# Optimization experiments

Measured on AMD Instinct MI355X. Metric: run time of the kernel, lower is better.

Reference implementation:

```python
import jax, jax.numpy as jnp
import numpy as np

EPS = 1e-6
NUM_HEADS = 16


def _layernorm(x, g, b):
    m = jnp.mean(x, axis=-1, keepdims=True)
    v = jnp.mean(jnp.square(x - m), axis=-1, keepdims=True)
    return (x - m) / jnp.sqrt(v + EPS) * g + b


def _rotate_half(x):
    x1, x2 = jnp.split(x, 2, axis=-1)
    return jnp.concatenate([-x2, x1], axis=-1)


def setup_inputs() -> dict:
    key = jax.random.key(0)
    B, N, C = 2, 2048, 1024
    H = NUM_HEADS
    D = C // H
    F = int(C * 4.0)
    ks = jax.random.split(key, 12)
    s = 0.02
    pos = jnp.arange(N)[:, None].astype(jnp.float32)
    inv_freq = 1.0 / (10000.0 ** (jnp.arange(0, D, 2, dtype=jnp.float32) / D))
    freqs = pos * inv_freq[None, :]          # [N, D/2]
    emb = jnp.concatenate([freqs, freqs], axis=-1)  # [N, D]
    return {
        "x": jax.random.normal(ks[0], (B, N, C), jnp.float32),
        "rotary_cos": jnp.cos(emb),
        "rotary_sin": jnp.sin(emb),
        "ln1_g": jnp.ones((C,), jnp.float32),
        "ln1_b": jnp.zeros((C,), jnp.float32),
        "Wq": jax.random.normal(ks[1], (C, C), jnp.float32) * s,
        "bq": jnp.zeros((C,), jnp.float32),
        "Wk": jax.random.normal(ks[2], (C, C), jnp.float32) * s,
        "bk": jnp.zeros((C,), jnp.float32),
        "Wv": jax.random.normal(ks[3], (C, C), jnp.float32) * s,
        "bv": jnp.zeros((C,), jnp.float32),
        "Wo": jax.random.normal(ks[4], (C, C), jnp.float32) * s,
        "bo": jnp.zeros((C,), jnp.float32),
        "ln2_g": jnp.ones((C,), jnp.float32),
        "ln2_b": jnp.zeros((C,), jnp.float32),
        "W1": jax.random.normal(ks[5], (F, C), jnp.float32) * s,
        "b1": jnp.zeros((F,), jnp.float32),
        "W2": jax.random.normal(ks[6], (C, F), jnp.float32) * s,
        "b2": jnp.zeros((C,), jnp.float32),
    }


def reference(x, rotary_cos, rotary_sin, ln1_g, ln1_b, Wq, bq, Wk, bk, Wv, bv,
              Wo, bo, ln2_g, ln2_b, W1, b1, W2, b2):
    B, N, C = x.shape
    H = NUM_HEADS
    D = C // H

    # --- attention branch ---
    h = _layernorm(x, ln1_g, ln1_b)
    q = (h @ Wq.T + bq).reshape(B, N, H, D).transpose(0, 2, 1, 3)  # [B,H,N,D]
    k = (h @ Wk.T + bk).reshape(B, N, H, D).transpose(0, 2, 1, 3)
    v = (h @ Wv.T + bv).reshape(B, N, H, D).transpose(0, 2, 1, 3)

    cos = rotary_cos[None, None, :, :]  # [1,1,N,D]
    sin = rotary_sin[None, None, :, :]
    q = q * cos + _rotate_half(q) * sin
    k = k * cos + _rotate_half(k) * sin

    scale = D ** -0.5
    attn = jnp.einsum('bhnd,bhmd->bhnm', q, k) * scale
    attn = jax.nn.softmax(attn, axis=-1)
    out = jnp.einsum('bhnm,bhmd->bhnd', attn, v)
    out = out.transpose(0, 2, 1, 3).reshape(B, N, C)
    out = out @ Wo.T + bo
    x = x + out

    # --- MLP branch ---
    h = _layernorm(x, ln2_g, ln2_b)
    h = jax.nn.gelu(h @ W1.T + b1, approximate=False)  # torch nn.GELU exact
    h = h @ W2.T + b2
    return x + h
```

## Files before the change

### kernel.cpp

```cpp
#include <hip/hip_runtime.h>
#include <hip/hip_bf16.h>

#define B_ 2
#define N_ 2048
#define C_ 1024
#define H_ 16
#define D_ 64
#define F_ 4096
#define M_ 4096

typedef __attribute__((ext_vector_type(8))) short bf16x8;
typedef __attribute__((ext_vector_type(4))) float f32x4;

__device__ inline unsigned short f2bf(float f) {
  unsigned int u = __float_as_uint(f);
  u = (u + 0x7FFFu + ((u >> 16) & 1u)) >> 16;
  return (unsigned short)u;
}

__global__ __launch_bounds__(256)
void cvt_all(const float4* __restrict__ s0, const float4* __restrict__ s1,
             const float4* __restrict__ s2, const float4* __restrict__ s3,
             const float4* __restrict__ s4, const float4* __restrict__ s5,
             ushort4* __restrict__ d0, ushort4* __restrict__ d1,
             ushort4* __restrict__ d2, ushort4* __restrict__ d3,
             ushort4* __restrict__ d4, ushort4* __restrict__ d5) {
  int b = blockIdx.x;
  const float4* s; ushort4* d; int i;
  if      (b < 1024) { s = s0; d = d0; i = b * 256 + threadIdx.x; }
  else if (b < 2048) { s = s1; d = d1; i = (b - 1024) * 256 + threadIdx.x; }
  else if (b < 3072) { s = s2; d = d2; i = (b - 2048) * 256 + threadIdx.x; }
  else if (b < 4096) { s = s3; d = d3; i = (b - 3072) * 256 + threadIdx.x; }
  else if (b < 8192) { s = s4; d = d4; i = (b - 4096) * 256 + threadIdx.x; }
  else               { s = s5; d = d5; i = (b - 8192) * 256 + threadIdx.x; }
  float4 f = s[i];
  ushort4 o;
  o.x = f2bf(f.x); o.y = f2bf(f.y); o.z = f2bf(f.z); o.w = f2bf(f.w);
  d[i] = o;
}

__global__ __launch_bounds__(256)
void ln_kernel(const float* __restrict__ x, const float* __restrict__ g,
               const float* __restrict__ b, unsigned short* __restrict__ out) {
  __shared__ float red[8];
  const int row = blockIdx.x;
  const int t = threadIdx.x;
  const float4 xv = *(const float4*)(x + row * 1024 + t * 4);
  float s  = xv.x + xv.y + xv.z + xv.w;
  float sq = xv.x * xv.x + xv.y * xv.y + xv.z * xv.z + xv.w * xv.w;
  #pragma unroll
  for (int off = 32; off >= 1; off >>= 1) {
    s  += __shfl_down(s, off);
    sq += __shfl_down(sq, off);
  }
  const int lane = t & 63, wave = t >> 6;
  if (lane == 0) { red[wave * 2] = s; red[wave * 2 + 1] = sq; }
  __syncthreads();
  float ts = red[0] + red[2] + red[4] + red[6];
  float tq = red[1] + red[3] + red[5] + red[7];
  float mean = ts * (1.0f / 1024.0f);
  float var  = tq * (1.0f / 1024.0f) - mean * mean;
  float rstd = rsqrtf(var + 1e-6f);
  float xs[4] = {xv.x, xv.y, xv.z, xv.w};
  #pragma unroll
  for (int i = 0; i < 4; i++) {
    int c = t * 4 + i;
    float y = (xs[i] - mean) * rstd * g[c] + b[c];
    out[row * 1024 + c] = f2bf(y);
  }
}

template<int MODE, int BN>
__global__ __launch_bounds__(256)
void gemm_bt(const unsigned short* __restrict__ A,
             const unsigned short* __restrict__ Bw,
             int K, int Nout, int npc,
             const float* __restrict__ bias,
             const float* __restrict__ resid,
             unsigned short* __restrict__ out_bf,
             float* __restrict__ out_f32) {
  constexpr int NJ = BN / 32;
  __shared__ unsigned short sA[128 * 64];
  __shared__ unsigned short sB[BN * 64];
  const int t = threadIdx.x;
  const int wave = t >> 6, lane = t & 63;
  const int quad = lane >> 4, l16 = lane & 15;
  const int wm = (wave & 1) * 64, wn = (wave >> 1) * (BN / 2);
  const int id = blockIdx.y * gridDim.x + blockIdx.x;
  const int xcd = id & 7, r_ = id >> 3;
  const int n_blk = xcd * npc + r_ % npc;
  const int m_blk = r_ / npc;
  const int m0 = m_blk * 128, n0 = n_blk * BN;

  f32x4 acc[4][NJ];
  #pragma unroll
  for (int i = 0; i < 4; i++)
    #pragma unroll
    for (int j = 0; j < NJ; j++) acc[i][j] = (f32x4){0.f, 0.f, 0.f, 0.f};

  const unsigned short* gA = A  + (m0 + (t >> 3)) * K + (t & 7) * 8;
  const unsigned short* gB = Bw + (n0 + (t >> 3)) * K + (t & 7) * 8;
  unsigned short* lA = &sA[(wave * 8) * 64];
  unsigned short* lB = &sB[(wave * 8) * 64];

  for (int k0 = 0; k0 < K; k0 += 64) {
    #pragma unroll
    for (int i = 0; i < 4; i++)
      __builtin_amdgcn_global_load_lds((const unsigned int*)(gA + (32 * i) * K + k0),
                                       (unsigned int*)(lA + 32 * i * 64), 16, 0, 0);
    #pragma unroll
    for (int i = 0; i < BN / 32; i++)
      __builtin_amdgcn_global_load_lds((const unsigned int*)(gB + (32 * i) * K + k0),
                                       (unsigned int*)(lB + 32 * i * 64), 16, 0, 0);
    __syncthreads();
    #pragma unroll
    for (int kk = 0; kk < 2; kk++) {
      bf16x8 af[4], bfr[NJ];
      #pragma unroll
      for (int i = 0; i < 4; i++)
        af[i] = *(const bf16x8*)(&sA[(wm + i * 16 + l16) * 64 + kk * 32 + quad * 8]);
      #pragma unroll
      for (int j = 0; j < NJ; j++)
        bfr[j] = *(const bf16x8*)(&sB[(wn + j * 16 + l16) * 64 + kk * 32 + quad * 8]);
      #pragma unroll
      for (int i = 0; i < 4; i++)
        #pragma unroll
        for (int j = 0; j < NJ; j++)
          acc[i][j] = __builtin_amdgcn_mfma_f32_16x16x32_bf16(af[i], bfr[j], acc[i][j], 0, 0, 0);
    }
    __syncthreads();
  }

  #pragma unroll
  for (int i = 0; i < 4; i++) {
    #pragma unroll
    for (int j = 0; j < NJ; j++) {
      int col = n0 + wn + j * 16 + l16;
      #pragma unroll
      for (int r = 0; r < 4; r++) {
        int row = m0 + wm + i * 16 + quad * 4 + r;
        float v = acc[i][j][r];
        if (MODE == 1 || MODE == 3) {
          out_f32[row * Nout + col] = v + bias[col] + resid[row * Nout + col];
        } else {
          v += bias[col];
          float w = v * (1.0f + 0.044715f * v * v);
          float gl = v / (1.0f + __expf(-1.5957691216f * w));
          out_bf[row * Nout + col] = f2bf(gl);
        }
      }
    }
  }
}

__global__ __launch_bounds__(256)
void gemm_qkv(const unsigned short* __restrict__ A,
              const unsigned short* __restrict__ Bw,
              const float* __restrict__ bq, const float* __restrict__ bk,
              const float* __restrict__ bv,
              const float* __restrict__ rc, const float* __restrict__ rs,
              unsigned short* __restrict__ qo, unsigned short* __restrict__ ko,
              unsigned short* __restrict__ vt) {
  const int K = C_;
  __shared__ unsigned short sA[128 * 64];
  __shared__ unsigned short sB[128 * 64];
  const int t = threadIdx.x;
  const int wave = t >> 6, lane = t & 63;
  const int quad = lane >> 4, l16 = lane & 15;
  const int wm = (wave & 1) * 64, wn = (wave >> 1) * 64;
  const int id = blockIdx.y * gridDim.x + blockIdx.x;
  const int xcd = id & 7, r_ = id >> 3;
  const int n_blk = xcd * 3 + r_ % 3;
  const int m_blk = r_ / 3;
  const int m0 = m_blk * 128, n0 = n_blk * 128;

  f32x4 acc[4][4];
  #pragma unroll
  for (int i = 0; i < 4; i++)
    #pragma unroll
    for (int j = 0; j < 4; j++) acc[i][j] = (f32x4){0.f, 0.f, 0.f, 0.f};

  const unsigned short* gA = A  + (m0 + (t >> 3)) * K + (t & 7) * 8;
  const unsigned short* gB = Bw + (n0 + (t >> 3)) * K + (t & 7) * 8;
  unsigned short* lA = &sA[(wave * 8) * 64];
  unsigned short* lB = &sB[(wave * 8) * 64];

  for (int k0 = 0; k0 < K; k0 += 64) {
    #pragma unroll
    for (int i = 0; i < 4; i++) {
      __builtin_amdgcn_global_load_lds((const unsigned int*)(gA + (32 * i) * K + k0),
                                       (unsigned int*)(lA + 32 * i * 64), 16, 0, 0);
      __builtin_amdgcn_global_load_lds((const unsigned int*)(gB + (32 * i) * K + k0),
                                       (unsigned int*)(lB + 32 * i * 64), 16, 0, 0);
    }
    __syncthreads();
    #pragma unroll
    for (int kk = 0; kk < 2; kk++) {
      bf16x8 af[4], bfr[4];
      #pragma unroll
      for (int i = 0; i < 4; i++)
        af[i] = *(const bf16x8*)(&sA[(wm + i * 16 + l16) * 64 + kk * 32 + quad * 8]);
      #pragma unroll
      for (int j = 0; j < 4; j++)
        bfr[j] = *(const bf16x8*)(&sB[(wn + j * 16 + l16) * 64 + kk * 32 + quad * 8]);
      #pragma unroll
      for (int i = 0; i < 4; i++)
        #pragma unroll
        for (int j = 0; j < 4; j++)
          acc[i][j] = __builtin_amdgcn_mfma_f32_16x16x32_bf16(af[i], bfr[j], acc[i][j], 0, 0, 0);
    }
    __syncthreads();
  }

  const int rgn = n_blk >> 3;
  const int c0 = (n_blk & 7) * 128;

  if (rgn == 2) {
    #pragma unroll
    for (int i = 0; i < 4; i++) {
      int row0 = m0 + wm + i * 16 + quad * 4;
      int bidx = row0 >> 11, n0r = row0 & 2047;
      #pragma unroll
      for (int j = 0; j < 4; j++) {
        int d = j * 16 + l16;
        int c = c0 + wn + d;
        int h = c >> 6;
        float bb = bv[c];
        __hip_bfloat162 p01 = __float22bfloat162_rn(float2{acc[i][j][0] + bb, acc[i][j][1] + bb});
        __hip_bfloat162 p23 = __float22bfloat162_rn(float2{acc[i][j][2] + bb, acc[i][j][3] + bb});
        unsigned int u01, u23;
        __builtin_memcpy(&u01, &p01, 4);
        __builtin_memcpy(&u23, &p23, 4);
        *(uint2*)(vt + (((bidx * 16 + h) * 64) + (c & 63)) * 2048 + n0r) = make_uint2(u01, u23);
      }
    }
  } else {
    const float* bias = (rgn == 0) ? bq : bk;
    unsigned short* outp = (rgn == 0) ? qo : ko;
    #pragma unroll
    for (int i = 0; i < 4; i++) {
      #pragma unroll
      for (int r = 0; r < 4; r++) {
        int row = m0 + wm + i * 16 + quad * 4 + r;
        int bidx = row >> 11, n = row & 2047;
        #pragma unroll
        for (int j = 0; j < 4; j++) {
          int d = j * 16 + l16;
          int c = c0 + wn + d;
          int h = c >> 6;
          int oi = ((bidx * 16 + h) * 2048 + n) * 64 + d;
          float val = acc[i][j][r] + bias[c];
          float pv  = acc[i][j ^ 2][r] + bias[c ^ 32];
          float rot = (j < 2) ? -pv : pv;
          float y = val * rc[n * 64 + d] + rot * rs[n * 64 + d];
          if (rgn == 0) y *= 0.125f;
          outp[oi] = f2bf(y);
        }
      }
    }
  }
}

__global__ __launch_bounds__(256)
void flash_attn(const unsigned short* __restrict__ q,
                const unsigned short* __restrict__ k,
                const unsigned short* __restrict__ vt,
                unsigned short* __restrict__ o) {
  __shared__ unsigned short sK[2][64 * 64];
  __shared__ unsigned short sVt[2][64 * 64];
  __shared__ unsigned short sPt[2][4][16 * 72];
  const int t = threadIdx.x;
  const int wave = t >> 6, lane = t & 63;
  const int quad = lane >> 4, l16 = lane & 15;
  const int id = blockIdx.y * gridDim.x + blockIdx.x;
  const int bh = (id & 7) * 4 + ((id >> 3) & 3);
  const int qb = id >> 5;
  const int base = bh * (N_ * D_);

  bf16x8 qa[2][2];
  #pragma unroll
  for (int qt = 0; qt < 2; qt++) {
    int qrow = qb * 128 + wave * 32 + qt * 16 + l16;
    #pragma unroll
    for (int kk = 0; kk < 2; kk++)
      qa[qt][kk] = *(const bf16x8*)(q + base + qrow * D_ + kk * 32 + quad * 8);
  }
  float l_i[2] = {0.f, 0.f};
  f32x4 o_acc[2][4];
  #pragma unroll
  for (int qt = 0; qt < 2; qt++)
    #pragma unroll
    for (int dt = 0; dt < 4; dt++) o_acc[qt][dt] = (f32x4){0.f, 0.f, 0.f, 0.f};

  const unsigned short* gK  = k  + base + (t >> 3) * 64 + (t & 7) * 8;
  const unsigned short* gVt = vt + bh * (64 * 2048) + (t >> 3) * 2048 + (t & 7) * 8;

  auto stage = [&](int kt, int buf) {
    unsigned short* lK = &sK[buf][(wave * 8) * 64];
    unsigned short* lV = &sVt[buf][(wave * 8) * 64];
    #pragma unroll
    for (int i = 0; i < 2; i++) {
      __builtin_amdgcn_global_load_lds((const unsigned int*)(gK + (kt * 64 + 32 * i) * 64),
                                       (unsigned int*)(lK + 32 * i * 64), 16, 0, 0);
      __builtin_amdgcn_global_load_lds((const unsigned int*)(gVt + 32 * i * 2048 + kt * 64),
                                       (unsigned int*)(lV + 32 * i * 64), 16, 0, 0);
    }
  };
  stage(0, 0);
  __syncthreads();

  for (int kt = 0; kt < N_ / 64; kt++) {
    const int cur = kt & 1;
    if (kt < N_ / 64 - 1) stage(kt + 1, cur ^ 1);

    f32x4 s_acc[2][4];
    #pragma unroll
    for (int nt = 0; nt < 4; nt++) {
      bf16x8 kb0 = *(const bf16x8*)(&sK[cur][(nt * 16 + l16) * 64 + quad * 8]);
      bf16x8 kb1 = *(const bf16x8*)(&sK[cur][(nt * 16 + l16) * 64 + 32 + quad * 8]);
      #pragma unroll
      for (int qt = 0; qt < 2; qt++) {
        f32x4 a = (f32x4){0.f, 0.f, 0.f, 0.f};
        a = __builtin_amdgcn_mfma_f32_16x16x32_bf16(kb0, qa[qt][0], a, 0, 0, 0);
        a = __builtin_amdgcn_mfma_f32_16x16x32_bf16(kb1, qa[qt][1], a, 0, 0, 0);
        s_acc[qt][nt] = a;
      }
    }
    #pragma unroll
    for (int qt = 0; qt < 2; qt++) {
      float rsum = 0.f;
      #pragma unroll
      for (int nt = 0; nt < 4; nt++)
        #pragma unroll
        for (int r = 0; r < 4; r++) {
          float p = __expf(s_acc[qt][nt][r]);
          s_acc[qt][nt][r] = p;
          rsum += p;
        }
      rsum += __shfl_xor(rsum, 16);
      rsum += __shfl_xor(rsum, 32);
      l_i[qt] += rsum;
      #pragma unroll
      for (int nt = 0; nt < 4; nt++) {
        __hip_bfloat162 p01 = __float22bfloat162_rn(float2{s_acc[qt][nt][0], s_acc[qt][nt][1]});
        __hip_bfloat162 p23 = __float22bfloat162_rn(float2{s_acc[qt][nt][2], s_acc[qt][nt][3]});
        unsigned int u01, u23;
        __builtin_memcpy(&u01, &p01, 4);
        __builtin_memcpy(&u23, &p23, 4);
        *(uint2*)(&sPt[qt][wave][l16 * 72 + nt * 16 + quad * 4]) = make_uint2(u01, u23);
      }
    }
    __asm__ volatile("s_waitcnt lgkmcnt(0)" ::: "memory");
    bf16x8 pt[2][2];
    #pragma unroll
    for (int qt = 0; qt < 2; qt++) {
      pt[qt][0] = *(const bf16x8*)(&sPt[qt][wave][l16 * 72 + quad * 8]);
      pt[qt][1] = *(const bf16x8*)(&sPt[qt][wave][l16 * 72 + 32 + quad * 8]);
    }
    #pragma unroll
    for (int dt = 0; dt < 4; dt++) {
      int d0 = dt * 16 + l16;
      bf16x8 va0 = *(const bf16x8*)(&sVt[cur][d0 * 64 + quad * 8]);
      bf16x8 va1 = *(const bf16x8*)(&sVt[cur][d0 * 64 + 32 + quad * 8]);
      #pragma unroll
      for (int qt = 0; qt < 2; qt++) {
        o_acc[qt][dt] = __builtin_amdgcn_mfma_f32_16x16x32_bf16(va0, pt[qt][0], o_acc[qt][dt], 0, 0, 0);
        o_acc[qt][dt] = __builtin_amdgcn_mfma_f32_16x16x32_bf16(va1, pt[qt][1], o_acc[qt][dt], 0, 0, 0);
      }
    }
    __syncthreads();
  }

  const int b = bh >> 4, h = bh & 15;
  #pragma unroll
  for (int qt = 0; qt < 2; qt++) {
    const float inv = 1.0f / l_i[qt];
    const int tok = b * N_ + qb * 128 + wave * 32 + qt * 16 + l16;
    #pragma unroll
    for (int dt = 0; dt < 4; dt++) {
      __hip_bfloat162 p01 = __float22bfloat162_rn(float2{o_acc[qt][dt][0] * inv, o_acc[qt][dt][1] * inv});
      __hip_bfloat162 p23 = __float22bfloat162_rn(float2{o_acc[qt][dt][2] * inv, o_acc[qt][dt][3] * inv});
      unsigned int u01, u23;
      __builtin_memcpy(&u01, &p01, 4);
      __builtin_memcpy(&u23, &p23, 4);
      int col = h * 64 + dt * 16 + quad * 4;
      *(uint2*)(o + tok * C_ + col) = make_uint2(u01, u23);
    }
  }
}

extern "C" void kernel_launch(void* const* d_in, const int* in_sizes, int n_in,
                              void* d_out, int out_size, void* d_ws, size_t ws_size,
                              hipStream_t stream) {
  const float* x   = (const float*)d_in[0];
  const float* rc  = (const float*)d_in[1];
  const float* rs  = (const float*)d_in[2];
  const float* g1  = (const float*)d_in[3];
  const float* be1 = (const float*)d_in[4];
  const float* Wq  = (const float*)d_in[5];
  const float* bq  = (const float*)d_in[6];
  const float* Wk  = (const float*)d_in[7];
  const float* bk  = (const float*)d_in[8];
  const float* Wv  = (const float*)d_in[9];
  const float* bv  = (const float*)d_in[10];
  const float* Wo  = (const float*)d_in[11];
  const float* bo  = (const float*)d_in[12];
  const float* g2  = (const float*)d_in[13];
  const float* be2 = (const float*)d_in[14];
  const float* W1  = (const float*)d_in[15];
  const float* b1m = (const float*)d_in[16];
  const float* W2  = (const float*)d_in[17];
  const float* b2m = (const float*)d_in[18];
  float* out = (float*)d_out;

  char* ws = (char*)d_ws;
  unsigned short* wqkv = (unsigned short*)(ws + 0);
  unsigned short* wo   = (unsigned short*)(ws + 6291456);
  unsigned short* w1   = (unsigned short*)(ws + 8388608);
  unsigned short* w2   = (unsigned short*)(ws + 16777216);
  unsigned short* h1   = (unsigned short*)(ws + 25165824);
  unsigned short* qa   = (unsigned short*)(ws + 33554432);
  unsigned short* ka   = (unsigned short*)(ws + 41943040);
  unsigned short* va   = (unsigned short*)(ws + 50331648);
  unsigned short* ao   = (unsigned short*)(ws + 58720256);
  float*          x1   = (float*)(ws + 67108864);
  unsigned short* u    = (unsigned short*)(ws + 33554432);

  cvt_all<<<12288, 256, 0, stream>>>(
      (const float4*)Wq, (const float4*)Wk, (const float4*)Wv, (const float4*)Wo,
      (const float4*)W1, (const float4*)W2,
      (ushort4*)wqkv, (ushort4*)(wqkv + 1048576), (ushort4*)(wqkv + 2097152),
      (ushort4*)wo, (ushort4*)w1, (ushort4*)w2);

  ln_kernel<<<4096, 256, 0, stream>>>(x, g1, be1, h1);
  gemm_qkv<<<dim3(24, 32), 256, 0, stream>>>(h1, wqkv, bq, bk, bv, rc, rs, qa, ka, va);
  flash_attn<<<dim3(16, 32), 256, 0, stream>>>(qa, ka, va, ao);
  gemm_bt<1, 64><<<dim3(16, 32), 256, 0, stream>>>(ao, wo, 1024, 1024, 2, bo, x, nullptr, x1);
  ln_kernel<<<4096, 256, 0, stream>>>(x1, g2, be2, h1);
  gemm_bt<2, 128><<<dim3(32, 32), 256, 0, stream>>>(h1, w1, 1024, 4096, 4, b1m, nullptr, u, nullptr);
  gemm_bt<3, 64><<<dim3(16, 32), 256, 0, stream>>>(u, w2, 4096, 1024, 2, b2m, x1, nullptr, out);
}
```

Before: 428.0 us.

## Double-buffer LDS tiles in GEMM kernels and narrow FC1 tile width

Both GEMM kernels now keep two LDS buffers and issue the global-to-LDS loads for the next K tile before computing on the current one, so memory latency overlaps MFMA work. The FC1 launch also moves from BN=128 to BN=64 with twice as many blocks. Double buffering doubles LDS use per block, which can lower occupancy. The remaining trailing __syncthreads is the only barrier left, so correctness depends on it covering both the read-after-write and write-after-read hazards between buffers. The async global_load_lds may also need an explicit vmcnt wait before the barrier.

```diff
diff --git a/kernel.cpp b/kernel.cpp
--- a/kernel.cpp
+++ b/kernel.cpp
@@ -80,8 +80,8 @@
              unsigned short* __restrict__ out_bf,
              float* __restrict__ out_f32) {
   constexpr int NJ = BN / 32;
-  __shared__ unsigned short sA[128 * 64];
-  __shared__ unsigned short sB[BN * 64];
+  __shared__ unsigned short sA[2][128 * 64];
+  __shared__ unsigned short sB[2][BN * 64];
   const int t = threadIdx.x;
   const int wave = t >> 6, lane = t & 63;
   const int quad = lane >> 4, l16 = lane & 15;
@@ -100,10 +100,10 @@
 
   const unsigned short* gA = A  + (m0 + (t >> 3)) * K + (t & 7) * 8;
   const unsigned short* gB = Bw + (n0 + (t >> 3)) * K + (t & 7) * 8;
-  unsigned short* lA = &sA[(wave * 8) * 64];
-  unsigned short* lB = &sB[(wave * 8) * 64];
-
-  for (int k0 = 0; k0 < K; k0 += 64) {
+
+  auto stage = [&](int k0, int buf) {
+    unsigned short* lA = &sA[buf][(wave * 8) * 64];
+    unsigned short* lB = &sB[buf][(wave * 8) * 64];
     #pragma unroll
     for (int i = 0; i < 4; i++)
       __builtin_amdgcn_global_load_lds((const unsigned int*)(gA + (32 * i) * K + k0),
@@ -112,16 +112,24 @@
     for (int i = 0; i < BN / 32; i++)
       __builtin_amdgcn_global_load_lds((const unsigned int*)(gB + (32 * i) * K + k0),
                                        (unsigned int*)(lB + 32 * i * 64), 16, 0, 0);
-    __syncthreads();
+  };
+
+  stage(0, 0);
+  __syncthreads();
+
+  const int nk = K >> 6;
+  for (int kt = 0; kt < nk; kt++) {
+    const int cur = kt & 1;
+    if (kt + 1 < nk) stage((kt + 1) * 64, cur ^ 1);
     #pragma unroll
     for (int kk = 0; kk < 2; kk++) {
       bf16x8 af[4], bfr[NJ];
       #pragma unroll
       for (int i = 0; i < 4; i++)
-        af[i] = *(const bf16x8*)(&sA[(wm + i * 16 + l16) * 64 + kk * 32 + quad * 8]);
+        af[i] = *(const bf16x8*)(&sA[cur][(wm + i * 16 + l16) * 64 + kk * 32 + quad * 8]);
       #pragma unroll
       for (int j = 0; j < NJ; j++)
-        bfr[j] = *(const bf16x8*)(&sB[(wn + j * 16 + l16) * 64 + kk * 32 + quad * 8]);
+        bfr[j] = *(const bf16x8*)(&sB[cur][(wn + j * 16 + l16) * 64 + kk * 32 + quad * 8]);
       #pragma unroll
       for (int i = 0; i < 4; i++)
         #pragma unroll
@@ -162,8 +170,8 @@
               unsigned short* __restrict__ qo, unsigned short* __restrict__ ko,
               unsigned short* __restrict__ vt) {
   const int K = C_;
-  __shared__ unsigned short sA[128 * 64];
-  __shared__ unsigned short sB[128 * 64];
+  __shared__ unsigned short sA[2][128 * 64];
+  __shared__ unsigned short sB[2][128 * 64];
   const int t = threadIdx.x;
   const int wave = t >> 6, lane = t & 63;
   const int quad = lane >> 4, l16 = lane & 15;
@@ -182,10 +190,10 @@
 
   const unsigned short* gA = A  + (m0 + (t >> 3)) * K + (t & 7) * 8;
   const unsigned short* gB = Bw + (n0 + (t >> 3)) * K + (t & 7) * 8;
-  unsigned short* lA = &sA[(wave * 8) * 64];
-  unsigned short* lB = &sB[(wave * 8) * 64];
-
-  for (int k0 = 0; k0 < K; k0 += 64) {
+
+  auto stage = [&](int k0, int buf) {
+    unsigned short* lA = &sA[buf][(wave * 8) * 64];
+    unsigned short* lB = &sB[buf][(wave * 8) * 64];
     #pragma unroll
     for (int i = 0; i < 4; i++) {
       __builtin_amdgcn_global_load_lds((const unsigned int*)(gA + (32 * i) * K + k0),
@@ -193,16 +201,24 @@
       __builtin_amdgcn_global_load_lds((const unsigned int*)(gB + (32 * i) * K + k0),
                                        (unsigned int*)(lB + 32 * i * 64), 16, 0, 0);
     }
-    __syncthreads();
+  };
+
+  stage(0, 0);
+  __syncthreads();
+
+  const int nk = K >> 6;
+  for (int kt = 0; kt < nk; kt++) {
+    const int cur = kt & 1;
+    if (kt + 1 < nk) stage((kt + 1) * 64, cur ^ 1);
     #pragma unroll
     for (int kk = 0; kk < 2; kk++) {
       bf16x8 af[4], bfr[4];
       #pragma unroll
       for (int i = 0; i < 4; i++)
-        af[i] = *(const bf16x8*)(&sA[(wm + i * 16 + l16) * 64 + kk * 32 + quad * 8]);
+        af[i] = *(const bf16x8*)(&sA[cur][(wm + i * 16 + l16) * 64 + kk * 32 + quad * 8]);
       #pragma unroll
       for (int j = 0; j < 4; j++)
-        bfr[j] = *(const bf16x8*)(&sB[(wn + j * 16 + l16) * 64 + kk * 32 + quad * 8]);
+        bfr[j] = *(const bf16x8*)(&sB[cur][(wn + j * 16 + l16) * 64 + kk * 32 + quad * 8]);
       #pragma unroll
       for (int i = 0; i < 4; i++)
         #pragma unroll
@@ -437,6 +453,6 @@
   flash_attn<<<dim3(16, 32), 256, 0, stream>>>(qa, ka, va, ao);
   gemm_bt<1, 64><<<dim3(16, 32), 256, 0, stream>>>(ao, wo, 1024, 1024, 2, bo, x, nullptr, x1);
   ln_kernel<<<4096, 256, 0, stream>>>(x1, g2, be2, h1);
-  gemm_bt<2, 128><<<dim3(32, 32), 256, 0, stream>>>(h1, w1, 1024, 4096, 4, b1m, nullptr, u, nullptr);
+  gemm_bt<2, 64><<<dim3(64, 32), 256, 0, stream>>>(h1, w1, 1024, 4096, 8, b1m, nullptr, u, nullptr);
   gemm_bt<3, 64><<<dim3(16, 32), 256, 0, stream>>>(u, w2, 4096, 1024, 2, b2m, x1, nullptr, out);
 }
```

New measurement: 428.2 us. About the same (+0.0%).
